# Kernel tuning notes

Measured on AMD Instinct MI355X. Metric: run time of the kernel, lower is better.

Reference implementation:

```python
import jax, jax.numpy as jnp
import numpy as np

B, T, F, H = 64, 512, 128, 512

def _rnn(x_seq, h0, Wih, Whh, bih, bhh):
    # PyTorch vanilla RNN: h_t = tanh(x_t @ Wih^T + bih + h_{t-1} @ Whh^T + bhh)
    def step(h, x_t):
        h = jnp.tanh(x_t @ Wih.T + bih + h @ Whh.T + bhh)
        return h, h
    _, ys = jax.lax.scan(step, h0, jnp.swapaxes(x_seq, 0, 1))  # scan over time
    return jnp.swapaxes(ys, 0, 1)  # [B, T, H]

def _decode(z, Wih, Whh, bih, bhh):
    # decoder input at step t = concat(prev_output, z_t); 1-layer RNN so prev_output == h_{t-1}
    def step(h, z_t):
        u = jnp.concatenate([h, z_t], axis=-1)  # [B, 2H]
        h_new = jnp.tanh(u @ Wih.T + bih + h @ Whh.T + bhh)
        return h_new, h_new
    h0 = jnp.zeros((z.shape[0], Whh.shape[0]), z.dtype)
    _, ys = jax.lax.scan(step, h0, jnp.swapaxes(z, 0, 1))
    return jnp.swapaxes(ys, 0, 1)  # [B, T, H]

def setup_inputs() -> dict:
    key = jax.random.key(0)
    ks = jax.random.split(key, 16)
    s = 0.02
    p = {
        'x':   jax.random.normal(ks[0], (B, T, F), jnp.float32),
        'eps': jax.random.normal(ks[1], (B, T, H), jnp.float32),
        'Wih_en': jax.random.normal(ks[2], (H, F)) * s,
        'Whh_en': jax.random.normal(ks[3], (H, H)) * s,
        'bih_en': jax.random.normal(ks[4], (H,)) * s,
        'bhh_en': jax.random.normal(ks[5], (H,)) * s,
        'W_mu':  jax.random.normal(ks[6], (H, H)) * s,
        'b_mu':  jax.random.normal(ks[7], (H,)) * s,
        'W_lv':  jax.random.normal(ks[8], (H, H)) * s,
        'b_lv':  jax.random.normal(ks[9], (H,)) * s,
        'Wih_de': jax.random.normal(ks[10], (H, 2 * H)) * s,
        'Whh_de': jax.random.normal(ks[11], (H, H)) * s,
        'bih_de': jax.random.normal(ks[12], (H,)) * s,
        'bhh_de': jax.random.normal(ks[13], (H,)) * s,
        'W_mux': jax.random.normal(ks[14], (F, H)) * s,
        'b_mux': jnp.zeros((F,)),
        'W_lvx': jax.random.normal(ks[15], (F, H)) * s,
        'b_lvx': jnp.zeros((F,)),
    }
    return p

def reference(x, eps, Wih_en, Whh_en, bih_en, bhh_en, W_mu, b_mu, W_lv, b_lv,
              Wih_de, Whh_de, bih_de, bhh_de, W_mux, b_mux, W_lvx, b_lvx):
    h0 = jnp.zeros((x.shape[0], Whh_en.shape[0]), x.dtype)
    y = _rnn(x, h0, Wih_en, Whh_en, bih_en, bhh_en)                 # [B,T,H]
    mu_post = y @ W_mu.T + b_mu
    logsigma2_post = y @ W_lv.T + b_lv
    z = eps * jnp.exp(logsigma2_post / 2) + mu_post                 # reparameterize
    outputs = _decode(z, Wih_de, Whh_de, bih_de, bhh_de)            # [B,T,H]
    mu_xhat = outputs @ W_mux.T + b_mux
    logsigma2_xhat = outputs @ W_lvx.T + b_lvx
    return (mu_post, logsigma2_post, mu_xhat, logsigma2_xhat)
```

## Files before the change

kernel.cpp:

```cpp
#include <hip/hip_runtime.h>

typedef _Float16 h2_t __attribute__((ext_vector_type(2)));
typedef _Float16 h4_t __attribute__((ext_vector_type(4)));
typedef _Float16 h8_t __attribute__((ext_vector_type(8)));
typedef float    f4_t __attribute__((ext_vector_type(4)));

#define B_  64
#define T_  512
#define F_  128
#define H_  512

static __device__ __forceinline__ int d4(int acc, unsigned a, unsigned b) {
#if __has_builtin(__builtin_amdgcn_sdot4)
    return __builtin_amdgcn_sdot4((int)a, (int)b, acc, false);
#else
    #pragma unroll
    for (int i = 0; i < 4; ++i)
        acc += (int)(signed char)((a >> (8 * i)) & 0xff) *
               (int)(signed char)((b >> (8 * i)) & 0xff);
    return acc;
#endif
}
static __device__ __forceinline__ int dot16i8(int acc, uint4 w, uint4 h) {
    acc = d4(acc, w.x, h.x);
    acc = d4(acc, w.y, h.y);
    acc = d4(acc, w.z, h.z);
    acc = d4(acc, w.w, h.w);
    return acc;
}

static __device__ __forceinline__ int pair_sum(int x) {
#if __has_builtin(__builtin_amdgcn_mov_dpp)
    return x + __builtin_amdgcn_mov_dpp(x, 0xB1, 0xF, 0xF, true);
#else
    return x + __shfl_xor(x, 1);
#endif
}

__global__ void k_cast_f16(const float* __restrict__ src, _Float16* __restrict__ dst, int n) {
    int i = blockIdx.x * blockDim.x + threadIdx.x;
    if (i < n) dst[i] = (_Float16)src[i];
}

__global__ void k_prep_z(const float* __restrict__ Wih_de, _Float16* __restrict__ Wz) {
    int i = blockIdx.x * blockDim.x + threadIdx.x;
    int cc = i >> 9, kk = i & 511;
    Wz[i] = (_Float16)Wih_de[cc * 1024 + 512 + kk];
}

__global__ void k_prep_bias(const float* __restrict__ a, const float* __restrict__ b,
                            float* __restrict__ o) {
    int i = threadIdx.x;
    o[i] = a[i] + b[i];
}

__global__ void k_cat2(const float* __restrict__ a, const float* __restrict__ b,
                       float* __restrict__ o, int n) {
    int i = blockIdx.x * blockDim.x + threadIdx.x;
    if (i < 2 * n) o[i] = (i < n) ? a[i] : b[i - n];
}

__global__ void k_quant(const float* __restrict__ A, int sA,
                        const float* __restrict__ Bo, int sB,
                        signed char* __restrict__ q, float* __restrict__ fac) {
    __shared__ float red[128];
    const int c = blockIdx.x, t = threadIdx.x;
    f4_t v = *(const f4_t*)(A + (size_t)c * sA + t * 4);
    if (Bo) {
        f4_t vb = *(const f4_t*)(Bo + (size_t)c * sB + t * 4);
        v = v + vb;
    }
    float m = fmaxf(fmaxf(fabsf(v[0]), fabsf(v[1])), fmaxf(fabsf(v[2]), fabsf(v[3])));
    red[t] = m;
    __syncthreads();
    for (int o = 64; o; o >>= 1) {
        if (t < o) red[t] = fmaxf(red[t], red[t + o]);
        __syncthreads();
    }
    float mx = red[0];
    float inv = mx > 0.f ? 127.f / mx : 0.f;
    unsigned r = 0;
    #pragma unroll
    for (int i = 0; i < 4; ++i) {
        int qi = (int)rintf(fminf(fmaxf(v[i] * inv, -127.f), 127.f));
        r |= ((unsigned)(unsigned char)(signed char)qi) << (8 * i);
    }
    *(unsigned*)(q + (size_t)c * 512 + t * 4) = r;
    if (t == 0) fac[c] = mx > 0.f ? mx / 127.f : 0.f;
}

#define BM 128
#define BN 128
#define BK 32
#define LDT 40

__global__ __launch_bounds__(256) void k_gemm(
    const _Float16* __restrict__ A, const _Float16* __restrict__ Bt,
    const float* __restrict__ bias,
    float* __restrict__ Cf, float* __restrict__ Cf2, _Float16* __restrict__ Ch,
    int M, int N, int nsplit, int K) {
    __shared__ _Float16 Al[BM * LDT];
    __shared__ _Float16 Bl[BN * LDT];
    const int tid = threadIdx.x;
    const int bm = blockIdx.x * BM, bn = blockIdx.y * BN;
    const int wid = tid >> 6, lane = tid & 63;
    const int wm = (wid >> 1) * 64, wn = (wid & 1) * 64;
    const int l15 = lane & 15, l4 = lane >> 4;

    f4_t acc[4][4];
    #pragma unroll
    for (int i = 0; i < 4; ++i)
        #pragma unroll
        for (int j = 0; j < 4; ++j) {
            f4_t zz = {0.f, 0.f, 0.f, 0.f};
            acc[i][j] = zz;
        }

    const int r = tid >> 1, hf = tid & 1;
    const h8_t* gA0 = (const h8_t*)(A + (size_t)(bm + r) * K);
    const h8_t* gB0 = (const h8_t*)(Bt + (size_t)(bn + r) * K);

    for (int k0 = 0; k0 < K; k0 += BK) {
        __syncthreads();
        int kf = (k0 >> 3) + hf * 2;
        h8_t a0 = gA0[kf], a1 = gA0[kf + 1];
        h8_t b0 = gB0[kf], b1 = gB0[kf + 1];
        *(h8_t*)&Al[r * LDT + hf * 16]     = a0;
        *(h8_t*)&Al[r * LDT + hf * 16 + 8] = a1;
        *(h8_t*)&Bl[r * LDT + hf * 16]     = b0;
        *(h8_t*)&Bl[r * LDT + hf * 16 + 8] = b1;
        __syncthreads();
        h8_t af[4], bf[4];
        #pragma unroll
        for (int i = 0; i < 4; ++i) af[i] = *(const h8_t*)&Al[(wm + i * 16 + l15) * LDT + l4 * 8];
        #pragma unroll
        for (int j = 0; j < 4; ++j) bf[j] = *(const h8_t*)&Bl[(wn + j * 16 + l15) * LDT + l4 * 8];
        #pragma unroll
        for (int i = 0; i < 4; ++i)
            #pragma unroll
            for (int j = 0; j < 4; ++j)
                acc[i][j] = __builtin_amdgcn_mfma_f32_16x16x32_f16(af[i], bf[j], acc[i][j], 0, 0, 0);
    }

    const int ns2 = N - nsplit;
    #pragma unroll
    for (int i = 0; i < 4; ++i) {
        int m0 = bm + wm + i * 16 + l4 * 4;
        #pragma unroll
        for (int j = 0; j < 4; ++j) {
            int n0 = bn + wn + j * 16 + l15;
            float bb = bias ? bias[n0] : 0.f;
            #pragma unroll
            for (int rr = 0; rr < 4; ++rr) {
                float v = acc[i][j][rr] + bb;
                if (Cf) {
                    if (n0 < nsplit) Cf[(size_t)(m0 + rr) * nsplit + n0] = v;
                    else             Cf2[(size_t)(m0 + rr) * ns2 + (n0 - nsplit)] = v;
                }
                if (Ch) Ch[(size_t)(m0 + rr) * N + n0] = (_Float16)v;
            }
        }
    }
}

__global__ __launch_bounds__(512) void k_rnn(
    const signed char* __restrict__ Wq,
    const float* __restrict__ fac,
    const _Float16* __restrict__ pre,
    _Float16* __restrict__ out) {
    __shared__ __align__(16) signed char h_q[2][H_];

    const int tid = threadIdx.x;
    const int half = tid & 1;
    const int r0 = tid & ~1;
    const int r1 = tid | 1;
    const int b = blockIdx.x;

    const uint4* q0 = (const uint4*)(Wq + (size_t)r0 * 512 + half * 256);
    const uint4* q1 = (const uint4*)(Wq + (size_t)r1 * 512 + half * 256);
    uint4 wa[16], wb[16];
    #pragma unroll
    for (int j = 0; j < 16; ++j) { wa[j] = q0[j]; wb[j] = q1[j]; }
    if (tid < 32) ((uint4*)&h_q[0][0])[tid] = make_uint4(0u, 0u, 0u, 0u);
    __syncthreads();

    const size_t base = (size_t)b * T_ * H_ + tid;
    float pcur = (float)pre[base];
    const float facr = fac[tid] * (1.f / 127.f);

    for (int t = 0; t < T_; ++t) {
        int tn = (t + 1 < T_) ? t + 1 : t;
        _Float16 pnx = pre[base + (size_t)tn * H_];

        int i0 = 0, i1 = 0;
        const uint4* hv = ((const uint4*)&h_q[t & 1][0]) + half * 16;
        #pragma unroll
        for (int j = 0; j < 16; ++j) {
            uint4 hh = hv[j];
            i0 = dot16i8(i0, wa[j], hh);
            i1 = dot16i8(i1, wb[j], hh);
        }

        int o0 = pair_sum(i0);
        int o1 = pair_sum(i1);
        int mine = half ? o1 : o0;

        float hn = tanhf((float)mine * facr + pcur);
        out[base + (size_t)t * H_] = (_Float16)hn;
        h_q[(t + 1) & 1][tid] = (signed char)(int)rintf(hn * 127.f);
        __syncthreads();
        pcur = (float)pnx;
    }
}

__global__ void k_z(const float* __restrict__ mu, const float* __restrict__ lv,
                    const float* __restrict__ eps, _Float16* __restrict__ z, int n4) {
    int i = blockIdx.x * blockDim.x + threadIdx.x;
    if (i >= n4) return;
    f4_t m = ((const f4_t*)mu)[i];
    f4_t l = ((const f4_t*)lv)[i];
    f4_t e = ((const f4_t*)eps)[i];
    h4_t r;
    #pragma unroll
    for (int j = 0; j < 4; ++j) r[j] = (_Float16)(e[j] * expf(l[j] * 0.5f) + m[j]);
    ((h4_t*)z)[i] = r;
}

extern "C" void kernel_launch(void* const* d_in, const int* in_sizes, int n_in,
                              void* d_out, int out_size, void* d_ws, size_t ws_size,
                              hipStream_t stream) {
    const float* x      = (const float*)d_in[0];
    const float* eps    = (const float*)d_in[1];
    const float* Wih_en = (const float*)d_in[2];
    const float* Whh_en = (const float*)d_in[3];
    const float* bih_en = (const float*)d_in[4];
    const float* bhh_en = (const float*)d_in[5];
    const float* W_mu   = (const float*)d_in[6];
    const float* b_mu   = (const float*)d_in[7];
    const float* W_lv   = (const float*)d_in[8];
    const float* b_lv   = (const float*)d_in[9];
    const float* Wih_de = (const float*)d_in[10];
    const float* Whh_de = (const float*)d_in[11];
    const float* bih_de = (const float*)d_in[12];
    const float* bhh_de = (const float*)d_in[13];
    const float* W_mux  = (const float*)d_in[14];
    const float* b_mux  = (const float*)d_in[15];
    const float* W_lvx  = (const float*)d_in[16];
    const float* b_lvx  = (const float*)d_in[17];
    float* out = (float*)d_out;

    char* ws = (char*)d_ws;
    _Float16* Wih_en_h = (_Float16*)(ws + 0);
    _Float16* W_mu_h   = (_Float16*)(ws + 655360);
    _Float16* W_lv_h   = (_Float16*)(ws + 1179648);
    _Float16* Wz_h     = (_Float16*)(ws + 1703936);
    _Float16* Wmux_h   = (_Float16*)(ws + 2752512);
    _Float16* Wlvx_h   = (_Float16*)(ws + 2883584);
    float*    benc     = (float*)(ws + 3014656);
    float*    bdec     = (float*)(ws + 3016704);
    signed char* Wq_en = (signed char*)(ws + 3018752);
    signed char* Wq_de = (signed char*)(ws + 3280896);
    float*    fac_en   = (float*)(ws + 3543040);
    float*    fac_de   = (float*)(ws + 3545088);
    float*    bmulv    = (float*)(ws + 3547136);
    float*    bmuxlvx  = (float*)(ws + 3551232);
    _Float16* x_h      = (_Float16*)(ws + 4194304);
    _Float16* pre_h    = (_Float16*)(ws + 12582912);
    _Float16* act_h    = (_Float16*)(ws + 46137344);
    _Float16* z_h      = (_Float16*)(ws + 79691776);

    const int thr = 256;
    k_cast_f16<<<(65536 + thr - 1) / thr, thr, 0, stream>>>(Wih_en, Wih_en_h, 65536);
    k_cast_f16<<<(262144 + thr - 1) / thr, thr, 0, stream>>>(W_mu, W_mu_h, 262144);
    k_cast_f16<<<(262144 + thr - 1) / thr, thr, 0, stream>>>(W_lv, W_lv_h, 262144);
    k_cast_f16<<<(65536 + thr - 1) / thr, thr, 0, stream>>>(W_mux, Wmux_h, 65536);
    k_cast_f16<<<(65536 + thr - 1) / thr, thr, 0, stream>>>(W_lvx, Wlvx_h, 65536);
    k_cast_f16<<<(4194304 + thr - 1) / thr, thr, 0, stream>>>(x, x_h, 4194304);
    k_prep_z<<<262144 / thr, thr, 0, stream>>>(Wih_de, Wz_h);
    k_prep_bias<<<1, 512, 0, stream>>>(bih_en, bhh_en, benc);
    k_prep_bias<<<1, 512, 0, stream>>>(bih_de, bhh_de, bdec);
    k_cat2<<<4, 256, 0, stream>>>(b_mu, b_lv, bmulv, 512);
    k_cat2<<<1, 256, 0, stream>>>(b_mux, b_lvx, bmuxlvx, 128);
    k_quant<<<512, 128, 0, stream>>>(Whh_en, 512, nullptr, 0, Wq_en, fac_en);
    k_quant<<<512, 128, 0, stream>>>(Wih_de, 1024, Whh_de, 512, Wq_de, fac_de);

    dim3 gFull(32768 / BM, 512 / BN);
    dim3 gWide(32768 / BM, 1024 / BN);
    dim3 gNarrow(32768 / BM, 256 / BN);

    k_gemm<<<gFull, 256, 0, stream>>>(x_h, Wih_en_h, benc, nullptr, nullptr, pre_h,
                                      32768, 512, 512, 128);
    k_rnn<<<64, 512, 0, stream>>>(Wq_en, fac_en, pre_h, act_h);
    k_gemm<<<gWide, 256, 0, stream>>>(act_h, W_mu_h, bmulv, out, out + 16777216, nullptr,
                                      32768, 1024, 512, 512);
    k_z<<<4194304 / thr, thr, 0, stream>>>(out, out + 16777216, eps, z_h, 4194304);
    k_gemm<<<gFull, 256, 0, stream>>>(z_h, Wz_h, bdec, nullptr, nullptr, pre_h,
                                      32768, 512, 512, 512);
    k_rnn<<<64, 512, 0, stream>>>(Wq_de, fac_de, pre_h, act_h);
    k_gemm<<<gNarrow, 256, 0, stream>>>(act_h, Wmux_h, bmuxlvx, out + 33554432, out + 37748736,
                                        nullptr, 32768, 256, 128, 512);
}
```

Baseline: 1.069 ms.

## Use int8 MFMA for RNN recurrence with repacked weights split across registers and LDS

The per-step matrix-vector product in the recurrent kernel now uses 16x16x64 int8 MFMA instructions instead of scalar sdot4 dot products. A new repack kernel lays the quantized recurrent weights out in MFMA A-operand fragment order. Each thread keeps 20 fragments in registers and the other 12 in shared memory. The MFMA diagonal results go through a shared buffer with an extra barrier per step, and tanhf is replaced by an exp-based fast tanh. The batch-of-one matvec wastes most MFMA columns, and the added LDS traffic and barrier may offset the gain on this latency-bound serial loop.

Measured after the change: 1.263 ms. 1.18x slower.

```diff
diff --git a/kernel.cpp b/kernel.cpp
--- a/kernel.cpp
+++ b/kernel.cpp
@@ -4,37 +4,18 @@
 typedef _Float16 h4_t __attribute__((ext_vector_type(4)));
 typedef _Float16 h8_t __attribute__((ext_vector_type(8)));
 typedef float    f4_t __attribute__((ext_vector_type(4)));
+typedef int      v4i  __attribute__((ext_vector_type(4)));
 
 #define B_  64
 #define T_  512
 #define F_  128
 #define H_  512
 
-static __device__ __forceinline__ int d4(int acc, unsigned a, unsigned b) {
-#if __has_builtin(__builtin_amdgcn_sdot4)
-    return __builtin_amdgcn_sdot4((int)a, (int)b, acc, false);
-#else
-    #pragma unroll
-    for (int i = 0; i < 4; ++i)
-        acc += (int)(signed char)((a >> (8 * i)) & 0xff) *
-               (int)(signed char)((b >> (8 * i)) & 0xff);
-    return acc;
-#endif
-}
-static __device__ __forceinline__ int dot16i8(int acc, uint4 w, uint4 h) {
-    acc = d4(acc, w.x, h.x);
-    acc = d4(acc, w.y, h.y);
-    acc = d4(acc, w.z, h.z);
-    acc = d4(acc, w.w, h.w);
-    return acc;
-}
-
-static __device__ __forceinline__ int pair_sum(int x) {
-#if __has_builtin(__builtin_amdgcn_mov_dpp)
-    return x + __builtin_amdgcn_mov_dpp(x, 0xB1, 0xF, 0xF, true);
-#else
-    return x + __shfl_xor(x, 1);
-#endif
+static __device__ __forceinline__ float tanh_fast(float x) {
+    float ax = fabsf(x);
+    float e = __expf(-2.f * ax);
+    float r = (1.f - e) * __frcp_rn(1.f + e);
+    return copysignf(r, x);
 }
 
 __global__ void k_cast_f16(const float* __restrict__ src, _Float16* __restrict__ dst, int n) {
@@ -87,6 +68,16 @@
     }
     *(unsigned*)(q + (size_t)c * 512 + t * 4) = r;
     if (t == 0) fac[c] = mx > 0.f ? mx / 127.f : 0.f;
+}
+
+__global__ void k_repack(const signed char* __restrict__ Wq, uint4* __restrict__ W5) {
+    int gid = blockIdx.x * blockDim.x + threadIdx.x;
+    int s = gid >> 9, tid2 = gid & 511;
+    int kt = s >> 2, rt = s & 3;
+    int w = tid2 >> 6, l = tid2 & 63;
+    int m = w * 64 + rt * 16 + (l & 15);
+    int k0 = kt * 64 + ((l >> 4) & 3) * 16;
+    W5[gid] = *(const uint4*)(Wq + (size_t)m * 512 + k0);
 }
 
 #define BM 128
@@ -164,48 +155,73 @@
 }
 
 __global__ __launch_bounds__(512) void k_rnn(
-    const signed char* __restrict__ Wq,
+    const uint4* __restrict__ W5,
     const float* __restrict__ fac,
     const _Float16* __restrict__ pre,
     _Float16* __restrict__ out) {
+    __shared__ __align__(16) uint4 WL[12 * 512];
     __shared__ __align__(16) signed char h_q[2][H_];
+    __shared__ __align__(16) int ipart[H_];
 
     const int tid = threadIdx.x;
-    const int half = tid & 1;
-    const int r0 = tid & ~1;
-    const int r1 = tid | 1;
     const int b = blockIdx.x;
-
-    const uint4* q0 = (const uint4*)(Wq + (size_t)r0 * 512 + half * 256);
-    const uint4* q1 = (const uint4*)(Wq + (size_t)r1 * 512 + half * 256);
-    uint4 wa[16], wb[16];
-    #pragma unroll
-    for (int j = 0; j < 16; ++j) { wa[j] = q0[j]; wb[j] = q1[j]; }
+    const int g16 = ((tid >> 4) & 3) * 16;
+
+    uint4 wa[20];
+    #pragma unroll
+    for (int s = 0; s < 20; ++s) wa[s] = W5[s * 512 + tid];
+    #pragma unroll
+    for (int s = 0; s < 12; ++s) WL[s * 512 + tid] = W5[(20 + s) * 512 + tid];
     if (tid < 32) ((uint4*)&h_q[0][0])[tid] = make_uint4(0u, 0u, 0u, 0u);
     __syncthreads();
 
     const size_t base = (size_t)b * T_ * H_ + tid;
     float pcur = (float)pre[base];
     const float facr = fac[tid] * (1.f / 127.f);
+    const bool diag = (tid & 15) == 0;
+    const int wrow = (tid >> 6) * 64 + ((tid >> 4) & 3) * 4;
 
     for (int t = 0; t < T_; ++t) {
         int tn = (t + 1 < T_) ? t + 1 : t;
         _Float16 pnx = pre[base + (size_t)tn * H_];
 
-        int i0 = 0, i1 = 0;
-        const uint4* hv = ((const uint4*)&h_q[t & 1][0]) + half * 16;
-        #pragma unroll
-        for (int j = 0; j < 16; ++j) {
-            uint4 hh = hv[j];
-            i0 = dot16i8(i0, wa[j], hh);
-            i1 = dot16i8(i1, wb[j], hh);
-        }
-
-        int o0 = pair_sum(i0);
-        int o1 = pair_sum(i1);
-        int mine = half ? o1 : o0;
-
-        float hn = tanhf((float)mine * facr + pcur);
+        v4i a0 = {0, 0, 0, 0}, a1 = {0, 0, 0, 0}, a2 = {0, 0, 0, 0}, a3 = {0, 0, 0, 0};
+        const signed char* hb = &h_q[t & 1][0];
+        #pragma unroll
+        for (int kt = 0; kt < 5; ++kt) {
+            v4i bf = *(const v4i*)(hb + kt * 64 + g16);
+            a0 = __builtin_amdgcn_mfma_i32_16x16x64_i8(
+                     __builtin_bit_cast(v4i, wa[kt * 4 + 0]), bf, a0, 0, 0, 0);
+            a1 = __builtin_amdgcn_mfma_i32_16x16x64_i8(
+                     __builtin_bit_cast(v4i, wa[kt * 4 + 1]), bf, a1, 0, 0, 0);
+            a2 = __builtin_amdgcn_mfma_i32_16x16x64_i8(
+                     __builtin_bit_cast(v4i, wa[kt * 4 + 2]), bf, a2, 0, 0, 0);
+            a3 = __builtin_amdgcn_mfma_i32_16x16x64_i8(
+                     __builtin_bit_cast(v4i, wa[kt * 4 + 3]), bf, a3, 0, 0, 0);
+        }
+        #pragma unroll
+        for (int kt = 5; kt < 8; ++kt) {
+            v4i bf = *(const v4i*)(hb + kt * 64 + g16);
+            int s0 = (kt - 5) * 4;
+            a0 = __builtin_amdgcn_mfma_i32_16x16x64_i8(
+                     __builtin_bit_cast(v4i, WL[(s0 + 0) * 512 + tid]), bf, a0, 0, 0, 0);
+            a1 = __builtin_amdgcn_mfma_i32_16x16x64_i8(
+                     __builtin_bit_cast(v4i, WL[(s0 + 1) * 512 + tid]), bf, a1, 0, 0, 0);
+            a2 = __builtin_amdgcn_mfma_i32_16x16x64_i8(
+                     __builtin_bit_cast(v4i, WL[(s0 + 2) * 512 + tid]), bf, a2, 0, 0, 0);
+            a3 = __builtin_amdgcn_mfma_i32_16x16x64_i8(
+                     __builtin_bit_cast(v4i, WL[(s0 + 3) * 512 + tid]), bf, a3, 0, 0, 0);
+        }
+
+        if (diag) {
+            *(v4i*)&ipart[wrow]      = a0;
+            *(v4i*)&ipart[wrow + 16] = a1;
+            *(v4i*)&ipart[wrow + 32] = a2;
+            *(v4i*)&ipart[wrow + 48] = a3;
+        }
+        __syncthreads();
+
+        float hn = tanh_fast((float)ipart[tid] * facr + pcur);
         out[base + (size_t)t * H_] = (_Float16)hn;
         h_q[(t + 1) & 1][tid] = (signed char)(int)rintf(hn * 127.f);
         __syncthreads();
@@ -264,6 +280,8 @@
     float*    fac_de   = (float*)(ws + 3545088);
     float*    bmulv    = (float*)(ws + 3547136);
     float*    bmuxlvx  = (float*)(ws + 3551232);
+    uint4*    W5_en    = (uint4*)(ws + 3552256);
+    uint4*    W5_de    = (uint4*)(ws + 3814400);
     _Float16* x_h      = (_Float16*)(ws + 4194304);
     _Float16* pre_h    = (_Float16*)(ws + 12582912);
     _Float16* act_h    = (_Float16*)(ws + 46137344);
@@ -283,6 +301,8 @@
     k_cat2<<<1, 256, 0, stream>>>(b_mux, b_lvx, bmuxlvx, 128);
     k_quant<<<512, 128, 0, stream>>>(Whh_en, 512, nullptr, 0, Wq_en, fac_en);
     k_quant<<<512, 128, 0, stream>>>(Wih_de, 1024, Whh_de, 512, Wq_de, fac_de);
+    k_repack<<<64, 256, 0, stream>>>(Wq_en, W5_en);
+    k_repack<<<64, 256, 0, stream>>>(Wq_de, W5_de);
 
     dim3 gFull(32768 / BM, 512 / BN);
     dim3 gWide(32768 / BM, 1024 / BN);
@@ -290,13 +310,13 @@
 
     k_gemm<<<gFull, 256, 0, stream>>>(x_h, Wih_en_h, benc, nullptr, nullptr, pre_h,
                                       32768, 512, 512, 128);
-    k_rnn<<<64, 512, 0, stream>>>(Wq_en, fac_en, pre_h, act_h);
+    k_rnn<<<64, 512, 0, stream>>>(W5_en, fac_en, pre_h, act_h);
     k_gemm<<<gWide, 256, 0, stream>>>(act_h, W_mu_h, bmulv, out, out + 16777216, nullptr,
                                       32768, 1024, 512, 512);
     k_z<<<4194304 / thr, thr, 0, stream>>>(out, out + 16777216, eps, z_h, 4194304);
     k_gemm<<<gFull, 256, 0, stream>>>(z_h, Wz_h, bdec, nullptr, nullptr, pre_h,
                                       32768, 512, 512, 512);
-    k_rnn<<<64, 512, 0, stream>>>(Wq_de, fac_de, pre_h, act_h);
+    k_rnn<<<64, 512, 0, stream>>>(W5_de, fac_de, pre_h, act_h);
     k_gemm<<<gNarrow, 256, 0, stream>>>(act_h, Wmux_h, bmuxlvx, out + 33554432, out + 37748736,
                                         nullptr, 32768, 256, 128, 512);
 }
```
